# Performance work log

Hardware: AMD Instinct MI355X
Metric: run time of the kernel (lower is better)

Reference implementation:

```python
import jax, jax.numpy as jnp
import numpy as np

# Constants describing the (equal-length) ragged batch and CRF tag space
B, L = 64, 512                 # 64 sequences of 512 segment-tokens each
C = 1024                       # fuse_embedding_channel
NUM_CLASSES = 5                # real field classes
NUM_TAGS = NUM_CLASSES + 2     # + START + STOP
START, STOP = NUM_CLASSES, NUM_CLASSES + 1
NEG = -10000.0


def setup_inputs() -> dict:
    key = jax.random.key(0)
    k1, k2, k3, k4 = jax.random.split(key, 4)
    fuse_embeddings = jax.random.normal(k1, (B * L, C), jnp.float32)
    label_class = jax.random.randint(k2, (B * L,), 0, NUM_CLASSES)
    # classification head params (Linear C -> NUM_TAGS)
    W = jax.random.normal(k3, (NUM_TAGS, C), jnp.float32) * 0.02
    b = jnp.zeros((NUM_TAGS,), jnp.float32)
    # CRF transition matrix: transitions[next, prev]
    transitions = jax.random.normal(k4, (NUM_TAGS, NUM_TAGS), jnp.float32) * 0.01
    transitions = transitions.at[START, :].set(NEG).at[:, STOP].set(NEG)
    return {"fuse_embeddings": fuse_embeddings, "label_class": label_class,
            "W": W, "b": b, "transitions": transitions}


def _crf_nll_sum(feats, tags, transitions):
    """Sum over batch of (forward_alg score - gold score).
    feats: [B, L, T] emissions, tags: [B, L] int, transitions: [T, T] (next, prev)."""
    # --- forward algorithm (batched log-sum-exp recurrence) ---
    init = jnp.full((B, NUM_TAGS), NEG, feats.dtype).at[:, START].set(0.0)

    def step(fv, emit):
        # fv: [B, prev], emit: [B, next]
        fv_new = jax.nn.logsumexp(fv[:, None, :] + transitions[None, :, :], axis=2) + emit
        return fv_new, None

    fv, _ = jax.lax.scan(step, init, jnp.swapaxes(feats, 0, 1))  # scan over L
    fwd_score = jax.nn.logsumexp(fv + transitions[STOP][None, :], axis=1)  # [B]

    # --- gold sentence score ---
    tags_ext = jnp.concatenate([jnp.full((B, 1), START, tags.dtype), tags], axis=1)
    emit_sc = jnp.take_along_axis(feats, tags[..., None], axis=2)[..., 0].sum(axis=1)
    trans_sc = transitions[tags_ext[:, 1:], tags_ext[:, :-1]].sum(axis=1)
    gold = emit_sc + trans_sc + transitions[STOP, tags[:, -1]]
    return (fwd_score - gold).sum()


def reference(fuse_embeddings, label_class, W, b, transitions):
    # per-token linear projection to tag logits
    pred_class = fuse_embeddings @ W.T + b          # [N, NUM_TAGS]
    feats = pred_class.reshape(B, L, NUM_TAGS)
    tags = label_class.reshape(B, L)
    score = _crf_nll_sum(feats, tags, transitions)
    return (jnp.reshape(score, (1,)), label_class.astype(jnp.int32), pred_class)
```

## Files before the change

kernel.cpp:

```cpp
#include <hip/hip_runtime.h>
#include <hip/hip_cooperative_groups.h>

namespace cg = cooperative_groups;

#define BSEQ 64
#define LSEQ 512
#define CCH  1024
#define NT   7
#define NC   5
#define NTOK (BSEQ*LSEQ)
#define START_TAG 5
#define STOP_TAG  6
#define NEGV (-10000.0f)
#define GRID_LOGITS 1024
#define FGRID 1024
#define FBLK  256

#define WS_M   0
#define WS_G   32768
#define WS_U   33792
#define WS_TOT 34304

typedef float vfloat4 __attribute__((ext_vector_type(4)));

template<int CTRL, int RMASK, int BMASK>
__device__ __forceinline__ float dpp_add(float x) {
    int y = __builtin_amdgcn_update_dpp(0, __float_as_int(x), CTRL, RMASK, BMASK, true);
    return x + __int_as_float(y);
}
__device__ __forceinline__ float wave_sum(float x) {
    x = dpp_add<0x111, 0xF, 0xF>(x);
    x = dpp_add<0x112, 0xF, 0xF>(x);
    x = dpp_add<0x114, 0xF, 0xF>(x);
    x = dpp_add<0x118, 0xF, 0xF>(x);
    x = dpp_add<0x142, 0xA, 0xF>(x);
    x = dpp_add<0x143, 0xC, 0xF>(x);
    return x;
}

__device__ __forceinline__ float lse5(const float v0, const float v1, const float v2,
                                      const float v3, const float v4) {
    float m = fmaxf(fmaxf(fmaxf(v0, v1), fmaxf(v2, v3)), v4);
    float s = __expf(v0 - m) + __expf(v1 - m) + __expf(v2 - m)
            + __expf(v3 - m) + __expf(v4 - m);
    return m + __logf(s);
}

__global__ __launch_bounds__(256)
void k_fused(const float* __restrict__ X, const float* __restrict__ W,
             const float* __restrict__ bvec, const int* __restrict__ lab,
             const float* __restrict__ trans, float* __restrict__ out,
             float* __restrict__ ws)
{
    __shared__ float Wl[NT][CCH];
    __shared__ float bl[NT];
    __shared__ float Tl[49];
    __shared__ float E_lds[32][5];
    __shared__ float Msub[4*25];
    __shared__ float Cb[2*25];
    __shared__ float Mbuf[16*25];

    const int tid  = threadIdx.x;
    const int lane = tid & 63;
    const int wv   = tid >> 6;
    const int bx   = blockIdx.x;

    if (bx == 0 && tid == 0) atomicExch(out, 0.0f);

    vfloat4 xb[3][4];
    const size_t rbase = (size_t)bx * 32 + wv;

    #define ISSUE_PHASE(p, slot)                                                    \
        if ((p) < 8) {                                                              \
            const int G_ = (p) >> 2, k_ = (p) & 3;                                  \
            _Pragma("unroll")                                                       \
            for (int j = 0; j < 4; j++) {                                           \
                const size_t row_ = rbase + (size_t)((G_*4 + j) * 4);               \
                const vfloat4* xp_ = (const vfloat4*)(X + row_ * CCH) + (k_*64 + lane); \
                xb[slot][j] = __builtin_nontemporal_load(xp_);                      \
            }                                                                       \
        }

    ISSUE_PHASE(0, 0)
    ISSUE_PHASE(1, 1)

    {
        const vfloat4* W4  = (const vfloat4*)W;
        vfloat4*       Wl4 = (vfloat4*)(&Wl[0][0]);
        for (int i = tid; i < NT*CCH/4; i += FBLK) Wl4[i] = W4[i];
        if (tid < NT) bl[tid] = bvec[tid];
        if (tid < 49) Tl[tid] = trans[tid];
        const int gidx = bx * FBLK + tid;
        if (gidx < NTOK) out[1 + gidx] = (float)lab[gidx];
    }
    __syncthreads();

    float* outP = out + 1 + NTOK;

    float acc[4][NT];
    #pragma unroll
    for (int j = 0; j < 4; j++)
        #pragma unroll
        for (int t = 0; t < NT; t++) acc[j][t] = 0.0f;

    #pragma unroll
    for (int p = 0; p < 8; ++p) {
        const int slot = p % 3;
        const int k    = p & 3;

        ISSUE_PHASE(p + 2, (p + 2) % 3)

        vfloat4 wreg[NT];
        {
            const int cb = (k*64 + lane) * 4;
            #pragma unroll
            for (int t = 0; t < NT; t++)
                wreg[t] = *(const vfloat4*)(&Wl[t][cb]);
        }

        #pragma unroll
        for (int j = 0; j < 4; j++) {
            #pragma unroll
            for (int t = 0; t < NT; t++) {
                acc[j][t] = fmaf(xb[slot][j].x, wreg[t].x,
                            fmaf(xb[slot][j].y, wreg[t].y,
                            fmaf(xb[slot][j].z, wreg[t].z,
                            fmaf(xb[slot][j].w, wreg[t].w, acc[j][t]))));
            }
        }

        if (k == 3) {
            const int G = p >> 2;
            #pragma unroll
            for (int j = 0; j < 4; j++) {
                const int m = G*4 + j;
                const size_t row = rbase + (size_t)(m * 4);
                const int rloc = wv + m*4;
                #pragma unroll
                for (int t = 0; t < NT; t++) {
                    float s = wave_sum(acc[j][t]);
                    if (lane == 63) {
                        const float e = s + bl[t];
                        outP[row * NT + t] = e;
                        if (t < NC) E_lds[rloc][t] = e;
                    }
                    acc[j][t] = 0.0f;
                }
            }
        }
    }
    #undef ISSUE_PHASE

    __syncthreads();

    const int sub = bx & 15;
    const int bat = bx >> 4;

    if (wv == 0) {
        if (lane < 20) {
            const int sc = lane / 5, basis = lane - sc*5;
            float TR[25];
            #pragma unroll
            for (int j = 0; j < NC; j++)
                #pragma unroll
                for (int k = 0; k < NC; k++) TR[j*5+k] = Tl[j*7+k];
            float fv[5];
            #pragma unroll
            for (int j = 0; j < NC; j++) fv[j] = (j == basis) ? 0.0f : NEGV;
            const int s0 = (sub == 0 && sc == 0) ? 1 : sc*8;
            const int s1 = sc*8 + 8;
            for (int s = s0; s < s1; ++s) {
                float fn[5];
                #pragma unroll
                for (int j = 0; j < NC; j++)
                    fn[j] = lse5(fv[0]+TR[j*5+0], fv[1]+TR[j*5+1], fv[2]+TR[j*5+2],
                                 fv[3]+TR[j*5+3], fv[4]+TR[j*5+4]) + E_lds[s][j];
                #pragma unroll
                for (int j = 0; j < NC; j++) fv[j] = fn[j];
            }
            #pragma unroll
            for (int j = 0; j < NC; j++) Msub[sc*25 + basis*5 + j] = fv[j];
        }
        if (lane < 50) {
            const int pp = lane / 25, r = lane - pp*25, i = r/5, jj = r - (r/5)*5;
            const float* A = &Msub[(2*pp)*25 + i*5];
            const float* B = &Msub[(2*pp+1)*25 + jj];
            Cb[pp*25 + r] = lse5(A[0]+B[0], A[1]+B[5], A[2]+B[10], A[3]+B[15], A[4]+B[20]);
        }
        if (lane < 25) {
            const int i = lane/5, jj = lane - i*5;
            const float* A = &Cb[i*5];
            const float* B = &Cb[25 + jj];
            ws[WS_M + (size_t)bx*32 + lane] =
                lse5(A[0]+B[0], A[1]+B[5], A[2]+B[10], A[3]+B[15], A[4]+B[20]);
        }
    } else if (wv == 1) {
        float g = 0.0f;
        if (lane < 32) {
            const int lg = bx*32 + lane;
            const int t  = lab[lg];
            const int tp = ((lg & (LSEQ-1)) == 0) ? START_TAG : lab[lg - 1];
            g = E_lds[lane][t] + Tl[t*7 + tp];
        }
        float gs = wave_sum(g);
        if (lane == 63) ws[WS_G + bx] = gs;
    } else if (wv == 2) {
        if (sub == 0 && lane < NC)
            ws[WS_U + bat*8 + lane] = Tl[lane*7 + START_TAG] + E_lds[0][lane];
    }

    __threadfence();
    cg::this_grid().sync();

    if (bx < BSEQ && wv == 0) {
        if (lane < 25) {
            #pragma unroll
            for (int m = 0; m < 16; ++m)
                Mbuf[m*25 + lane] = ws[WS_M + ((size_t)bx*16 + m)*32 + lane];
        }
        float gp = (lane < 16) ? ws[WS_G + bx*16 + lane] : 0.0f;
        float gtot = wave_sum(gp);
        gtot = __shfl(gtot, 63);
        if (lane < NC) {
            const int j = lane;
            float fvr = ws[WS_U + bx*8 + j];
            for (int m = 0; m < 16; ++m) {
                const float f0 = __shfl(fvr, 0), f1 = __shfl(fvr, 1), f2 = __shfl(fvr, 2),
                            f3 = __shfl(fvr, 3), f4 = __shfl(fvr, 4);
                const float* M = &Mbuf[m*25];
                fvr = lse5(f0 + M[0*5+j], f1 + M[1*5+j], f2 + M[2*5+j],
                           f3 + M[3*5+j], f4 + M[4*5+j]);
            }
            const float v0 = __shfl(fvr, 0), v1 = __shfl(fvr, 1), v2 = __shfl(fvr, 2),
                        v3 = __shfl(fvr, 3), v4 = __shfl(fvr, 4);
            if (j == 0) {
                float fwd = lse5(v0 + Tl[STOP_TAG*7+0], v1 + Tl[STOP_TAG*7+1],
                                 v2 + Tl[STOP_TAG*7+2], v3 + Tl[STOP_TAG*7+3],
                                 v4 + Tl[STOP_TAG*7+4]);
                float gold = gtot + Tl[STOP_TAG*7 + lab[bx*LSEQ + LSEQ - 1]];
                atomicAdd(out, fwd - gold);
            }
        }
    }
}

__global__ __launch_bounds__(256)
void k_logits(const float* __restrict__ X, const float* __restrict__ W,
              const float* __restrict__ bvec, const int* __restrict__ lab,
              float* __restrict__ out)
{
    __shared__ float Wl[NT][CCH];
    __shared__ float bl[NT];

    const int lane = threadIdx.x & 63;
    const int wid  = (blockIdx.x * 256 + threadIdx.x) >> 6;
    const int nw   = (GRID_LOGITS * 256) >> 6;

    vfloat4 xb[3][4];

    #define ISSUE_PHASE(p, slot)                                                   \
        if ((p) < 8) {                                                             \
            const int G_ = (p) >> 2, k_ = (p) & 3;                                 \
            _Pragma("unroll")                                                      \
            for (int j = 0; j < 4; j++) {                                          \
                const size_t row_ = (size_t)(wid + (G_*4 + j) * nw);               \
                const vfloat4* xp_ = (const vfloat4*)(X + row_ * CCH) + (k_*64 + lane); \
                xb[slot][j] = __builtin_nontemporal_load(xp_);                     \
            }                                                                      \
        }

    ISSUE_PHASE(0, 0)
    ISSUE_PHASE(1, 1)

    {
        const vfloat4* W4  = (const vfloat4*)W;
        vfloat4*       Wl4 = (vfloat4*)(&Wl[0][0]);
        for (int i = threadIdx.x; i < NT*CCH/4; i += 256) Wl4[i] = W4[i];
        if (threadIdx.x < NT) bl[threadIdx.x] = bvec[threadIdx.x];
    }
    __syncthreads();

    float* outP = out + 1 + NTOK;

    float acc[4][NT];
    #pragma unroll
    for (int j = 0; j < 4; j++)
        #pragma unroll
        for (int t = 0; t < NT; t++) acc[j][t] = 0.0f;

    #pragma unroll
    for (int p = 0; p < 8; ++p) {
        const int slot = p % 3;
        const int k    = p & 3;

        ISSUE_PHASE(p + 2, (p + 2) % 3)

        vfloat4 wreg[NT];
        {
            const int cb = (k*64 + lane) * 4;
            #pragma unroll
            for (int t = 0; t < NT; t++)
                wreg[t] = *(const vfloat4*)(&Wl[t][cb]);
        }

        #pragma unroll
        for (int j = 0; j < 4; j++) {
            #pragma unroll
            for (int t = 0; t < NT; t++) {
                acc[j][t] = fmaf(xb[slot][j].x, wreg[t].x,
                            fmaf(xb[slot][j].y, wreg[t].y,
                            fmaf(xb[slot][j].z, wreg[t].z,
                            fmaf(xb[slot][j].w, wreg[t].w, acc[j][t]))));
            }
        }

        if (k == 3) {
            const int G = p >> 2;
            #pragma unroll
            for (int j = 0; j < 4; j++) {
                const size_t row = (size_t)(wid + (G*4 + j) * nw);
                #pragma unroll
                for (int t = 0; t < NT; t++) {
                    float s = wave_sum(acc[j][t]);
                    if (lane == 63) outP[row * NT + t] = s + bl[t];
                    acc[j][t] = 0.0f;
                }
            }
        }
    }
    #undef ISSUE_PHASE

    for (int i = blockIdx.x * 256 + threadIdx.x; i < NTOK; i += GRID_LOGITS * 256)
        out[1 + i] = (float)lab[i];
    if (blockIdx.x == 0 && threadIdx.x == 0) out[0] = 0.0f;
}

__global__ __launch_bounds__(320)
void k_crf(const float* __restrict__ dout_ro, const int* __restrict__ lab,
           const float* __restrict__ trans, float* __restrict__ score)
{
    __shared__ float E[LSEQ*NT];
    __shared__ float M2[32*25];
    __shared__ float T[49];
    __shared__ float u_sh[NC];
    __shared__ float gred[5];

    const int b   = blockIdx.x;
    const int tid = threadIdx.x;
    const float* feats = dout_ro + 1 + NTOK + (size_t)b * (LSEQ*NT);

    for (int i = tid; i < LSEQ*NT; i += 320) E[i] = feats[i];
    if (tid < 49) T[tid] = trans[tid];
    __syncthreads();

    if (tid < NC) u_sh[tid] = T[tid*NT + START_TAG] + E[tid];

    float g = 0.0f;
    for (int l = tid; l < LSEQ; l += 320) {
        const int t  = lab[b*LSEQ + l];
        const int tp = (l == 0) ? START_TAG : lab[b*LSEQ + l - 1];
        g += E[l*NT + t] + T[t*NT + tp];
    }
    if (tid == 0) g += T[STOP_TAG*NT + lab[b*LSEQ + LSEQ - 1]];
    {
        float gs = wave_sum(g);
        if ((tid & 63) == 63) gred[tid >> 6] = gs;
    }

    float TR[NC*NC];
    #pragma unroll
    for (int j = 0; j < NC; j++)
        #pragma unroll
        for (int k = 0; k < NC; k++) TR[j*NC + k] = T[j*NT + k];

    const int chunk = tid / NC;
    const int basis = tid - chunk * NC;
    float fv[NC];
    #pragma unroll
    for (int j = 0; j < NC; j++) fv[j] = (j == basis) ? 0.0f : NEGV;

    const int l0    = (chunk == 0) ? 1 : chunk * 8;
    const int steps = (chunk == 0) ? 7 : 8;
    for (int s = 0; s < steps; s++) {
        const int l = l0 + s;
        float fn[NC];
        #pragma unroll
        for (int j = 0; j < NC; j++) {
            fn[j] = lse5(fv[0] + TR[j*NC+0], fv[1] + TR[j*NC+1], fv[2] + TR[j*NC+2],
                         fv[3] + TR[j*NC+3], fv[4] + TR[j*NC+4]) + E[l*NT + j];
        }
        #pragma unroll
        for (int j = 0; j < NC; j++) fv[j] = fn[j];
    }
    __syncthreads();
    #pragma unroll
    for (int j = 0; j < NC; j++) E[chunk*25 + basis*NC + j] = fv[j];

    int n = 64, cur = 0;
    while (n > 1) {
        __syncthreads();
        const float* in = (cur == 0) ? (const float*)E : (const float*)M2;
        float*       ob = (cur == 0) ? M2 : E;
        const int half = n >> 1;
        for (int e2 = tid; e2 < half*25; e2 += 320) {
            const int p = e2 / 25, r = e2 - p*25;
            const int i = r / NC, j = r - (r/NC)*NC;
            const float* A  = in + (2*p)*25 + i*NC;
            const float* Bm = in + (2*p + 1)*25 + j;
            ob[p*25 + r] = lse5(A[0] + Bm[0], A[1] + Bm[NC], A[2] + Bm[2*NC],
                                A[3] + Bm[3*NC], A[4] + Bm[4*NC]);
        }
        cur ^= 1; n = half;
    }
    __syncthreads();

    if (tid == 0) {
        float gg = gred[0] + gred[1] + gred[2] + gred[3] + gred[4];
        const float* M = (cur == 0) ? (const float*)E : (const float*)M2;
        float v[NC];
        #pragma unroll
        for (int j = 0; j < NC; j++)
            v[j] = lse5(u_sh[0] + M[0*NC+j], u_sh[1] + M[1*NC+j], u_sh[2] + M[2*NC+j],
                        u_sh[3] + M[3*NC+j], u_sh[4] + M[4*NC+j]);
        float fwd = lse5(v[0] + T[STOP_TAG*NT+0], v[1] + T[STOP_TAG*NT+1],
                         v[2] + T[STOP_TAG*NT+2], v[3] + T[STOP_TAG*NT+3],
                         v[4] + T[STOP_TAG*NT+4]);
        atomicAdd(score, fwd - gg);
    }
}

extern "C" void kernel_launch(void* const* d_in, const int* in_sizes, int n_in,
                              void* d_out, int out_size, void* d_ws, size_t ws_size,
                              hipStream_t stream) {
    const float* X     = (const float*)d_in[0];
    const int*   lab   = (const int*)  d_in[1];
    const float* W     = (const float*)d_in[2];
    const float* bvec  = (const float*)d_in[3];
    const float* trans = (const float*)d_in[4];
    float* out = (float*)d_out;
    float* wsf = (float*)d_ws;

    int maxB = 0;
    hipError_t oe = hipOccupancyMaxActiveBlocksPerMultiprocessor(&maxB, k_fused, FBLK, 0);
    if (oe == hipSuccess && maxB >= 4 && wsf != nullptr &&
        ws_size >= (size_t)WS_TOT * sizeof(float)) {
        void* kargs[] = {(void*)&X, (void*)&W, (void*)&bvec, (void*)&lab,
                         (void*)&trans, (void*)&out, (void*)&wsf};
        hipError_t le = hipLaunchCooperativeKernel((const void*)k_fused,
                                                   dim3(FGRID), dim3(FBLK),
                                                   kargs, 0, stream);
        if (le == hipSuccess) return;
    }

    k_logits<<<GRID_LOGITS, 256, 0, stream>>>(X, W, bvec, lab, out);
    k_crf<<<BSEQ, 320, 0, stream>>>(out, lab, trans, out);
}
```

Before: 211.7 us.

## Replace cooperative grid sync with per-sequence flag-based producer/consumer handoff

Drops the cooperative launch and its grid-wide barrier, and launches the fused kernel normally. Each block publishes its partial CRF matrices through atomic stores and sets a magic flag. The first block of each sequence spins on its 16 producer flags and reduces their chunks, then block 0 spins on the 64 per-sequence flags and writes the final sum. This avoids the grid-sync and cooperative-launch overhead but depends on consumer blocks not starving producers, since nothing guarantees co-residency. It also adds atomic traffic on the workspace.

```diff
diff --git a/kernel.cpp b/kernel.cpp
--- a/kernel.cpp
+++ b/kernel.cpp
@@ -1,7 +1,4 @@
 #include <hip/hip_runtime.h>
-#include <hip/hip_cooperative_groups.h>
-
-namespace cg = cooperative_groups;
 
 #define BSEQ 64
 #define LSEQ 512
@@ -15,13 +12,30 @@
 #define GRID_LOGITS 1024
 #define FGRID 1024
 #define FBLK  256
+#define MAGIC 0x5A17C0DEu
 
 #define WS_M   0
 #define WS_G   32768
 #define WS_U   33792
-#define WS_TOT 34304
+#define WS_PS  34304
+#define WS_CF  34368
+#define WS_FF  35392
+#define WS_TOT 35456
 
 typedef float vfloat4 __attribute__((ext_vector_type(4)));
+
+__device__ __forceinline__ void ws_store(float* p, float v) {
+    atomicExch((unsigned int*)p, __float_as_uint(v));
+}
+__device__ __forceinline__ float ws_load(float* p) {
+    return __uint_as_float(atomicAdd((unsigned int*)p, 0u));
+}
+__device__ __forceinline__ unsigned flag_read(float* p) {
+    return atomicAdd((unsigned int*)p, 0u);
+}
+__device__ __forceinline__ void flag_write(float* p, unsigned v) {
+    atomicExch((unsigned int*)p, v);
+}
 
 template<int CTRL, int RMASK, int BMASK>
 __device__ __forceinline__ float dpp_add(float x) {
@@ -58,14 +72,13 @@
     __shared__ float E_lds[32][5];
     __shared__ float Msub[4*25];
     __shared__ float Cb[2*25];
-    __shared__ float Mbuf[16*25];
 
     const int tid  = threadIdx.x;
     const int lane = tid & 63;
     const int wv   = tid >> 6;
     const int bx   = blockIdx.x;
-
-    if (bx == 0 && tid == 0) atomicExch(out, 0.0f);
+    const int sub  = bx & 15;
+    const int bat  = bx >> 4;
 
     vfloat4 xb[3][4];
     const size_t rbase = (size_t)bx * 32 + wv;
@@ -153,9 +166,6 @@
 
     __syncthreads();
 
-    const int sub = bx & 15;
-    const int bat = bx >> 4;
-
     if (wv == 0) {
         if (lane < 20) {
             const int sc = lane / 5, basis = lane - sc*5;
@@ -191,8 +201,8 @@
             const int i = lane/5, jj = lane - i*5;
             const float* A = &Cb[i*5];
             const float* B = &Cb[25 + jj];
-            ws[WS_M + (size_t)bx*32 + lane] =
-                lse5(A[0]+B[0], A[1]+B[5], A[2]+B[10], A[3]+B[15], A[4]+B[20]);
+            ws_store(&ws[WS_M + (size_t)bx*32 + lane],
+                     lse5(A[0]+B[0], A[1]+B[5], A[2]+B[10], A[3]+B[15], A[4]+B[20]));
         }
     } else if (wv == 1) {
         float g = 0.0f;
@@ -203,44 +213,68 @@
             g = E_lds[lane][t] + Tl[t*7 + tp];
         }
         float gs = wave_sum(g);
-        if (lane == 63) ws[WS_G + bx] = gs;
+        if (lane == 63) ws_store(&ws[WS_G + bx], gs);
     } else if (wv == 2) {
         if (sub == 0 && lane < NC)
-            ws[WS_U + bat*8 + lane] = Tl[lane*7 + START_TAG] + E_lds[0][lane];
-    }
-
-    __threadfence();
-    cg::this_grid().sync();
-
-    if (bx < BSEQ && wv == 0) {
-        if (lane < 25) {
-            #pragma unroll
-            for (int m = 0; m < 16; ++m)
-                Mbuf[m*25 + lane] = ws[WS_M + ((size_t)bx*16 + m)*32 + lane];
-        }
-        float gp = (lane < 16) ? ws[WS_G + bx*16 + lane] : 0.0f;
+            ws_store(&ws[WS_U + bat*8 + lane], Tl[lane*7 + START_TAG] + E_lds[0][lane]);
+    }
+
+    __syncthreads();
+    if (tid == 0) {
+        __threadfence();
+        flag_write(&ws[WS_CF + bx], MAGIC);
+    }
+
+    if (sub == 0 && wv == 0) {
+        if (lane < 16) {
+            while (flag_read(&ws[WS_CF + bat*16 + lane]) != MAGIC)
+                __builtin_amdgcn_s_sleep(8);
+            flag_write(&ws[WS_CF + bat*16 + lane], 0u);
+        }
+        __threadfence();
+
+        float Mm[16];
+        #pragma unroll
+        for (int m = 0; m < 16; ++m)
+            Mm[m] = (lane < 25) ? ws_load(&ws[WS_M + ((size_t)bat*16 + m)*32 + lane]) : 0.0f;
+
+        float gp = (lane < 16) ? ws_load(&ws[WS_G + bat*16 + lane]) : 0.0f;
         float gtot = wave_sum(gp);
         gtot = __shfl(gtot, 63);
-        if (lane < NC) {
-            const int j = lane;
-            float fvr = ws[WS_U + bx*8 + j];
-            for (int m = 0; m < 16; ++m) {
-                const float f0 = __shfl(fvr, 0), f1 = __shfl(fvr, 1), f2 = __shfl(fvr, 2),
-                            f3 = __shfl(fvr, 3), f4 = __shfl(fvr, 4);
-                const float* M = &Mbuf[m*25];
-                fvr = lse5(f0 + M[0*5+j], f1 + M[1*5+j], f2 + M[2*5+j],
-                           f3 + M[3*5+j], f4 + M[4*5+j]);
-            }
-            const float v0 = __shfl(fvr, 0), v1 = __shfl(fvr, 1), v2 = __shfl(fvr, 2),
-                        v3 = __shfl(fvr, 3), v4 = __shfl(fvr, 4);
-            if (j == 0) {
-                float fwd = lse5(v0 + Tl[STOP_TAG*7+0], v1 + Tl[STOP_TAG*7+1],
-                                 v2 + Tl[STOP_TAG*7+2], v3 + Tl[STOP_TAG*7+3],
-                                 v4 + Tl[STOP_TAG*7+4]);
-                float gold = gtot + Tl[STOP_TAG*7 + lab[bx*LSEQ + LSEQ - 1]];
-                atomicAdd(out, fwd - gold);
-            }
-        }
+
+        float fvr = (lane < NC) ? ws_load(&ws[WS_U + bat*8 + lane]) : 0.0f;
+        #pragma unroll
+        for (int m = 0; m < 16; ++m) {
+            const float f0 = __shfl(fvr, 0), f1 = __shfl(fvr, 1), f2 = __shfl(fvr, 2),
+                        f3 = __shfl(fvr, 3), f4 = __shfl(fvr, 4);
+            const float t0 = __shfl(Mm[m], 0*5 + lane);
+            const float t1 = __shfl(Mm[m], 1*5 + lane);
+            const float t2 = __shfl(Mm[m], 2*5 + lane);
+            const float t3 = __shfl(Mm[m], 3*5 + lane);
+            const float t4 = __shfl(Mm[m], 4*5 + lane);
+            fvr = lse5(f0 + t0, f1 + t1, f2 + t2, f3 + t3, f4 + t4);
+        }
+        const float v0 = __shfl(fvr, 0), v1 = __shfl(fvr, 1), v2 = __shfl(fvr, 2),
+                    v3 = __shfl(fvr, 3), v4 = __shfl(fvr, 4);
+        if (lane == 0) {
+            float fwd = lse5(v0 + Tl[STOP_TAG*7+0], v1 + Tl[STOP_TAG*7+1],
+                             v2 + Tl[STOP_TAG*7+2], v3 + Tl[STOP_TAG*7+3],
+                             v4 + Tl[STOP_TAG*7+4]);
+            float gold = gtot + Tl[STOP_TAG*7 + lab[bat*LSEQ + LSEQ - 1]];
+            ws_store(&ws[WS_PS + bat], fwd - gold);
+            __threadfence();
+            flag_write(&ws[WS_FF + bat], MAGIC);
+        }
+    }
+
+    if (bx == 0 && wv == 0) {
+        while (flag_read(&ws[WS_FF + lane]) != MAGIC)
+            __builtin_amdgcn_s_sleep(8);
+        flag_write(&ws[WS_FF + lane], 0u);
+        __threadfence();
+        float ps = ws_load(&ws[WS_PS + lane]);
+        float tot = wave_sum(ps);
+        if (lane == 63) out[0] = tot;
     }
 }
 
@@ -440,16 +474,9 @@
     float* out = (float*)d_out;
     float* wsf = (float*)d_ws;
 
-    int maxB = 0;
-    hipError_t oe = hipOccupancyMaxActiveBlocksPerMultiprocessor(&maxB, k_fused, FBLK, 0);
-    if (oe == hipSuccess && maxB >= 4 && wsf != nullptr &&
-        ws_size >= (size_t)WS_TOT * sizeof(float)) {
-        void* kargs[] = {(void*)&X, (void*)&W, (void*)&bvec, (void*)&lab,
-                         (void*)&trans, (void*)&out, (void*)&wsf};
-        hipError_t le = hipLaunchCooperativeKernel((const void*)k_fused,
-                                                   dim3(FGRID), dim3(FBLK),
-                                                   kargs, 0, stream);
-        if (le == hipSuccess) return;
+    if (wsf != nullptr && ws_size >= (size_t)WS_TOT * sizeof(float)) {
+        k_fused<<<FGRID, FBLK, 0, stream>>>(X, W, bvec, lab, trans, out, wsf);
+        return;
     }
 
     k_logits<<<GRID_LOGITS, 256, 0, stream>>>(X, W, bvec, lab, out);
```

After: 282.8 us. 33.6% more time.
